# Optimization experiments

Measured on AMD Instinct MI355X. Metric: run time of the kernel, lower is better.

## Reference

```python
import jax, jax.numpy as jnp
import numpy as np

D_MODEL = 1024
NHEAD = 16
HEAD_DIM = D_MODEL // NHEAD


def setup_inputs() -> dict:
    key = jax.random.key(0)
    ks = jax.random.split(key, 9)
    s = 0.02
    x = jax.random.normal(ks[0], (2, 2048, D_MODEL), dtype=jnp.float32)
    Wq = jax.random.normal(ks[1], (D_MODEL, D_MODEL), dtype=jnp.float32) * s
    bq = jnp.zeros((D_MODEL,), jnp.float32)
    Wk = jax.random.normal(ks[2], (D_MODEL, D_MODEL), dtype=jnp.float32) * s
    bk = jnp.zeros((D_MODEL,), jnp.float32)
    Wv = jax.random.normal(ks[3], (D_MODEL, D_MODEL), dtype=jnp.float32) * s
    bv = jnp.zeros((D_MODEL,), jnp.float32)
    Wo = jax.random.normal(ks[4], (D_MODEL, D_MODEL), dtype=jnp.float32) * s
    bo = jnp.zeros((D_MODEL,), jnp.float32)
    return {"x": x, "Wq": Wq, "bq": bq, "Wk": Wk, "bk": bk,
            "Wv": Wv, "bv": bv, "Wo": Wo, "bo": bo}


def _rope(x, sin, cos):
    # x: [B, L, H, Dh]; rotate-half as in the torch module
    half = x.shape[-1] // 2
    x1, x2 = x[..., :half], x[..., half:]
    rotated = jnp.concatenate([-x2, x1], axis=-1)
    return x * cos + rotated * sin


def reference(x, Wq, bq, Wk, bk, Wv, bv, Wo, bo):
    B, L, D = x.shape
    H, Dh = NHEAD, HEAD_DIM
    q = (x @ Wq.T + bq).reshape(B, L, H, Dh)
    k = (x @ Wk.T + bk).reshape(B, L, H, Dh)
    v = (x @ Wv.T + bv).reshape(B, L, H, Dh)

    inv_freq = 1.0 / (10000.0 ** (jnp.arange(0, Dh, 2, dtype=jnp.float32) / Dh))
    t = jnp.arange(L, dtype=jnp.float32)
    freqs = jnp.einsum('i,j->ij', t, inv_freq)          # [L, Dh/2]
    emb = jnp.concatenate([freqs, freqs], axis=-1)      # [L, Dh]
    cos = jnp.cos(emb)[None, :, None, :]
    sin = jnp.sin(emb)[None, :, None, :]

    q = _rope(q, sin, cos)
    k = _rope(k, sin, cos)

    # [B, H, L, L]
    scores = jnp.einsum('bqhd,bkhd->bhqk', q, k) / jnp.sqrt(jnp.float32(Dh))
    attn = jax.nn.softmax(scores, axis=-1)
    # dropout in eval mode = identity (p given as 0.0)
    out = jnp.einsum('bhqk,bkhd->bqhd', attn, v).reshape(B, L, D)
    return out @ Wo.T + bo
```

## Files before the change

kernel.cpp:

```cpp
#include <hip/hip_runtime.h>
#include <math.h>

#define D_MODEL 1024
#define NHEAD 16
#define HEAD_DIM 64
#define L_SEQ 2048
#define BATCH 2
#define M_ROWS 4096
#define SC_Q 0.18033688011112042f

typedef __attribute__((ext_vector_type(8))) short short8;
typedef __attribute__((ext_vector_type(4))) float floatx4;
typedef __attribute__((ext_vector_type(2))) __fp16 half2_t;
typedef __attribute__((ext_vector_type(4))) __fp16 half4_t;
typedef __attribute__((ext_vector_type(8))) __fp16 half8_t;

#if __has_builtin(__builtin_amdgcn_exp2f)
#define EXP2F(x) __builtin_amdgcn_exp2f(x)
#else
#define EXP2F(x) exp2f(x)
#endif

__device__ inline unsigned f2bf_u(float x) {
    unsigned u = __float_as_uint(x);
    return (u + 0x7fffu + ((u >> 16) & 1u)) >> 16;
}

__device__ inline void gl_lds16(const void* g, void* l) {
    __builtin_amdgcn_global_load_lds((const __attribute__((address_space(1))) void*)g,
                                     (__attribute__((address_space(3))) void*)l, 16, 0, 0);
}

__device__ inline void permlane16_swap(unsigned& a, unsigned& b) {
#if __has_builtin(__builtin_amdgcn_permlane16_swap)
    auto r = __builtin_amdgcn_permlane16_swap(a, b, false, false);
    a = r[0];
    b = r[1];
#else
    asm("v_permlane16_swap_b32 %0, %1" : "+v"(a), "+v"(b));
#endif
}

__global__ __launch_bounds__(256) void cvt_all(
    const float* __restrict__ x,  const float* __restrict__ wq,
    const float* __restrict__ wk, const float* __restrict__ wv,
    const float* __restrict__ wo,
    unsigned short* __restrict__ xb,  unsigned short* __restrict__ wqb,
    unsigned short* __restrict__ wkb, unsigned short* __restrict__ wvb,
    unsigned short* __restrict__ wob, float* __restrict__ rt) {
    if (blockIdx.y == 5) {
        for (int idx = blockIdx.x * 256 + threadIdx.x; idx < L_SEQ * 16;
             idx += gridDim.x * 256) {
            int l = idx >> 4, f = idx & 15;
            float if0 = (float)pow(10000.0, -(double)f / 32.0);
            float if1 = (float)pow(10000.0, -(double)(f + 16) / 32.0);
            float s0, c0, s1, c1;
            sincosf((float)l * if0, &s0, &c0);
            sincosf((float)l * if1, &s1, &c1);
            float4 v = {c0, c1, s0, s1};
            *(float4*)(rt + (size_t)idx * 4) = v;
        }
        return;
    }
    const float* s; unsigned short* d; int n;
    switch (blockIdx.y) {
        case 0:  s = x;  d = xb;  n = M_ROWS * D_MODEL; break;
        case 1:  s = wq; d = wqb; n = D_MODEL * D_MODEL; break;
        case 2:  s = wk; d = wkb; n = D_MODEL * D_MODEL; break;
        case 3:  s = wv; d = wvb; n = D_MODEL * D_MODEL; break;
        default: s = wo; d = wob; n = D_MODEL * D_MODEL; break;
    }
    int stride = gridDim.x * 256 * 4;
    for (int i = (blockIdx.x * 256 + threadIdx.x) * 4; i < n; i += stride) {
        float4 v = *(const float4*)(s + i);
        ushort4 o;
        o.x = (unsigned short)f2bf_u(v.x);
        o.y = (unsigned short)f2bf_u(v.y);
        o.z = (unsigned short)f2bf_u(v.z);
        o.w = (unsigned short)f2bf_u(v.w);
        *(ushort4*)(d + i) = o;
    }
}

__global__ __launch_bounds__(256, 3) void gemm_qkv(
    const unsigned short* __restrict__ xb,
    const unsigned short* __restrict__ wqb, const unsigned short* __restrict__ wkb,
    const unsigned short* __restrict__ wvb,
    const float* __restrict__ bq, const float* __restrict__ bk,
    const float* __restrict__ bv, const float* __restrict__ rt,
    unsigned short* __restrict__ qo, unsigned short* __restrict__ ko,
    unsigned short* __restrict__ vo) {
    __shared__ __align__(16) unsigned short As[128 * 64];
    __shared__ __align__(16) unsigned short Bs[128 * 64];

    const int K = D_MODEL;
    const int tid = threadIdx.x;
    const int lane = tid & 63;
    const int w = tid >> 6;
    const int quad = lane >> 4;
    const int wm = (w & 1) * 64;
    const int wn = (w >> 1) * 64;
    const int m0 = blockIdx.x * 128;
    const int n0 = blockIdx.y * 128;

    const unsigned short* Wsel; const float* bsel;
    unsigned short* osel; int mode; float oscale;
    if (blockIdx.z == 0)      { Wsel = wqb; bsel = bq; osel = qo; mode = 1; oscale = SC_Q; }
    else if (blockIdx.z == 1) { Wsel = wkb; bsel = bk; osel = ko; mode = 1; oscale = 1.0f; }
    else                      { Wsel = wvb; bsel = bv; osel = vo; mode = 2; oscale = 1.0f; }

    floatx4 acc[4][4];
#pragma unroll
    for (int i = 0; i < 4; ++i)
#pragma unroll
        for (int j = 0; j < 4; ++j) acc[i][j] = (floatx4){0.f, 0.f, 0.f, 0.f};

    const int sr8 = lane >> 3;
    const int ss8 = lane & 7;
    const unsigned short* Ag = xb + (size_t)m0 * K;
    const unsigned short* Bg = Wsel + (size_t)n0 * K;

    for (int k0 = 0; k0 < K; k0 += 64) {
        __syncthreads();
#pragma unroll
        for (int t = 0; t < 4; ++t) {
            int R0 = t * 32 + w * 8;
            int r = R0 + sr8;
            int c = ss8 ^ (r & 7);
            gl_lds16(Ag + (size_t)r * K + k0 + c * 8, (void*)(As + R0 * 64));
            gl_lds16(Bg + (size_t)r * K + k0 + c * 8, (void*)(Bs + R0 * 64));
        }
        __syncthreads();

#pragma unroll
        for (int ks = 0; ks < 2; ++ks) {
            short8 af[4], bf[4];
#pragma unroll
            for (int mt = 0; mt < 4; ++mt) {
                int ar = wm + mt * 16 + (lane & 15);
                int slot = (ks * 4 + quad) ^ (ar & 7);
                af[mt] = *(const short8*)(As + ar * 64 + slot * 8);
            }
#pragma unroll
            for (int nt = 0; nt < 4; ++nt) {
                int br = wn + nt * 16 + (lane & 15);
                int slot = (ks * 4 + quad) ^ (br & 7);
                bf[nt] = *(const short8*)(Bs + br * 64 + slot * 8);
            }
#pragma unroll
            for (int mt = 0; mt < 4; ++mt)
#pragma unroll
                for (int nt = 0; nt < 4; ++nt)
                    acc[mt][nt] = __builtin_amdgcn_mfma_f32_16x16x32_bf16(
                        af[mt], bf[nt], acc[mt][nt], 0, 0, 0);
        }
    }

#pragma unroll
    for (int nt = 0; nt < 4; ++nt) {
        float bn = bsel[n0 + wn + nt * 16 + (lane & 15)];
#pragma unroll
        for (int mt = 0; mt < 4; ++mt)
#pragma unroll
            for (int i = 0; i < 4; ++i) acc[mt][nt][i] += bn;
    }

    const int h = (n0 + wn) >> 6;

    if (mode == 1) {
#pragma unroll
        for (int mt = 0; mt < 4; ++mt)
#pragma unroll
            for (int i = 0; i < 4; ++i) {
                int m = m0 + wm + mt * 16 + (lane >> 4) * 4 + i;
                int b = m >> 11, l = m & (L_SEQ - 1);
                float4 tc = *(const float4*)(rt + ((size_t)(l * 16 + (lane & 15)) << 2));
#pragma unroll
                for (int nt = 0; nt < 4; ++nt) {
                    int dh = nt * 16 + (lane & 15);
                    float partner = acc[mt][nt ^ 2][i];
                    float rot = (nt < 2) ? -partner : partner;
                    float c = (nt & 1) ? tc.y : tc.x;
                    float s = (nt & 1) ? tc.w : tc.z;
                    float val = (acc[mt][nt][i] * c + rot * s) * oscale;
                    size_t idx = (((size_t)(b * NHEAD + h)) * L_SEQ + l) * HEAD_DIM + dh;
                    osel[idx] = (unsigned short)f2bf_u(val);
                }
            }
    } else {
#pragma unroll
        for (int mt = 0; mt < 4; ++mt)
#pragma unroll
            for (int ih = 0; ih < 4; ih += 2) {
                int m = m0 + wm + mt * 16 + (lane >> 4) * 4 + ih;
                int b = m >> 11, l = m & (L_SEQ - 1);
#pragma unroll
                for (int nt = 0; nt < 4; ++nt) {
                    int dh = nt * 16 + (lane & 15);
                    union { half2_t h; unsigned u; } cv;
                    cv.h = __builtin_amdgcn_cvt_pkrtz(acc[mt][nt][ih], acc[mt][nt][ih + 1]);
                    size_t idx = (((size_t)(b * NHEAD + h)) * HEAD_DIM + dh) * L_SEQ + l;
                    *(unsigned*)(vo + idx) = cv.u;
                }
            }
    }
}

__global__ __launch_bounds__(256) void gemm_out(
    const unsigned short* __restrict__ A, const unsigned short* __restrict__ Wb,
    const float* __restrict__ bias, float* __restrict__ out) {
    __shared__ __align__(16) unsigned short As[64 * 64];
    __shared__ __align__(16) unsigned short Bs[128 * 64];

    const int K = D_MODEL;
    const int tid = threadIdx.x;
    const int lane = tid & 63;
    const int w = tid >> 6;
    const int quad = lane >> 4;
    const int wm = (w & 1) * 32;
    const int wn = (w >> 1) * 64;
    const int m0 = blockIdx.x * 64;
    const int n0 = blockIdx.y * 128;

    floatx4 acc[2][4];
#pragma unroll
    for (int i = 0; i < 2; ++i)
#pragma unroll
        for (int j = 0; j < 4; ++j) acc[i][j] = (floatx4){0.f, 0.f, 0.f, 0.f};

    const int sr8 = lane >> 3;
    const int ss8 = lane & 7;
    const unsigned short* Ag = A + (size_t)m0 * K;
    const unsigned short* Bg = Wb + (size_t)n0 * K;

    for (int k0 = 0; k0 < K; k0 += 64) {
        __syncthreads();
#pragma unroll
        for (int t = 0; t < 2; ++t) {
            int R0 = t * 32 + w * 8;
            int r = R0 + sr8;
            int c = ss8 ^ (r & 7);
            gl_lds16(Ag + (size_t)r * K + k0 + c * 8, (void*)(As + R0 * 64));
        }
#pragma unroll
        for (int t = 0; t < 4; ++t) {
            int R0 = t * 32 + w * 8;
            int r = R0 + sr8;
            int c = ss8 ^ (r & 7);
            gl_lds16(Bg + (size_t)r * K + k0 + c * 8, (void*)(Bs + R0 * 64));
        }
        __syncthreads();

        short8 af[2][2], bf[4][2];
#pragma unroll
        for (int mt = 0; mt < 2; ++mt) {
            int ar = wm + mt * 16 + (lane & 15);
#pragma unroll
            for (int ks = 0; ks < 2; ++ks) {
                int slot = (ks * 4 + quad) ^ (ar & 7);
                af[mt][ks] = *(const short8*)(As + ar * 64 + slot * 8);
            }
        }
#pragma unroll
        for (int nt = 0; nt < 4; ++nt) {
            int br = wn + nt * 16 + (lane & 15);
#pragma unroll
            for (int ks = 0; ks < 2; ++ks) {
                int slot = (ks * 4 + quad) ^ (br & 7);
                bf[nt][ks] = *(const short8*)(Bs + br * 64 + slot * 8);
            }
        }
#pragma unroll
        for (int ks = 0; ks < 2; ++ks)
#pragma unroll
            for (int mt = 0; mt < 2; ++mt)
#pragma unroll
                for (int nt = 0; nt < 4; ++nt)
                    acc[mt][nt] = __builtin_amdgcn_mfma_f32_16x16x32_bf16(
                        af[mt][ks], bf[nt][ks], acc[mt][nt], 0, 0, 0);
    }

#pragma unroll
    for (int nt = 0; nt < 4; ++nt) {
        int n = n0 + wn + nt * 16 + (lane & 15);
        float bn = bias[n];
#pragma unroll
        for (int mt = 0; mt < 2; ++mt)
#pragma unroll
            for (int i = 0; i < 4; ++i) {
                int m = m0 + wm + mt * 16 + (lane >> 4) * 4 + i;
                out[(size_t)m * D_MODEL + n] = acc[mt][nt][i] + bn;
            }
    }
}

__global__ __launch_bounds__(256, 4) void attn_mfma(
    const unsigned short* __restrict__ q, const unsigned short* __restrict__ k,
    const unsigned short* __restrict__ vt,
    unsigned short* __restrict__ ao) {
    __shared__ __align__(16) unsigned short Ks[128 * 64];
    __shared__ __align__(16) unsigned short Vs[64 * 128];

    const int tid = threadIdx.x;
    const int lane = tid & 63;
    const int w = tid >> 6;
    const int quad = lane >> 4;
    const int ln = lane & 15;

    const int GX = L_SEQ / 64;
    int lin = blockIdx.y * GX + blockIdx.x;
    lin = (lin & 7) * 128 + (lin >> 3);
    const int q0 = (lin & (GX - 1)) * 64;
    const int bh = lin >> 5;

    const unsigned short* qb = q + (size_t)bh * L_SEQ * HEAD_DIM;
    const unsigned short* kb = k + (size_t)bh * L_SEQ * HEAD_DIM;
    const unsigned short* vb = vt + (size_t)bh * HEAD_DIM * L_SEQ;

    short8 qf[2];
#pragma unroll
    for (int ks = 0; ks < 2; ++ks)
        qf[ks] = *(const short8*)(
            qb + (size_t)(q0 + w * 16 + ln) * HEAD_DIM + ks * 32 + quad * 8);

    floatx4 o[4];
    floatx4 ls;
    ls = (floatx4){0.f, 0.f, 0.f, 0.f};
#pragma unroll
    for (int j = 0; j < 4; ++j) o[j] = (floatx4){0.f, 0.f, 0.f, 0.f};

    half8_t ones8;
#pragma unroll
    for (int j = 0; j < 8; ++j) ones8[j] = (__fp16)1.0f;

    const int srk = lane >> 3;
    const int ssk = lane & 7;
    const int srv = lane >> 4;
    const int ssv = lane & 15;
    const int pb = ((quad & 1) << 1) | (quad >> 1);

    for (int t = 0; t < L_SEQ / 128; ++t) {
        const int kv0 = t * 128;
        __syncthreads();
#pragma unroll
        for (int tt = 0; tt < 4; ++tt) {
            {
                int R0 = tt * 32 + w * 8;
                int r = R0 + srk;
                int c = ssk ^ (r & 7);
                gl_lds16(kb + (size_t)(kv0 + r) * HEAD_DIM + c * 8, (void*)(Ks + R0 * 64));
            }
            {
                int R0 = tt * 16 + w * 4;
                int r = R0 + srv;
                int c = ssv ^ (r & 15);
                gl_lds16(vb + (size_t)r * L_SEQ + kv0 + c * 8, (void*)(Vs + R0 * 128));
            }
        }
        __syncthreads();

#pragma unroll
        for (int mt2 = 0; mt2 < 4; ++mt2) {
            floatx4 s0 = (floatx4){0.f, 0.f, 0.f, 0.f};
            floatx4 s1 = (floatx4){0.f, 0.f, 0.f, 0.f};
            {
                int ar = mt2 * 32 + ln;
                short8 kf0 = *(const short8*)(Ks + ar * 64 + ((quad) ^ (ar & 7)) * 8);
                short8 kf1 = *(const short8*)(Ks + ar * 64 + ((4 + quad) ^ (ar & 7)) * 8);
                s0 = __builtin_amdgcn_mfma_f32_16x16x32_bf16(kf0, qf[0], s0, 0, 0, 0);
                s0 = __builtin_amdgcn_mfma_f32_16x16x32_bf16(kf1, qf[1], s0, 0, 0, 0);
            }
            {
                int ar = mt2 * 32 + 16 + ln;
                short8 kf0 = *(const short8*)(Ks + ar * 64 + ((quad) ^ (ar & 7)) * 8);
                short8 kf1 = *(const short8*)(Ks + ar * 64 + ((4 + quad) ^ (ar & 7)) * 8);
                s1 = __builtin_amdgcn_mfma_f32_16x16x32_bf16(kf0, qf[0], s1, 0, 0, 0);
                s1 = __builtin_amdgcn_mfma_f32_16x16x32_bf16(kf1, qf[1], s1, 0, 0, 0);
            }

            half8_t vf[4];
#pragma unroll
            for (int ntd = 0; ntd < 4; ++ntd) {
                int row = ntd * 16 + ln;
                int slot = (mt2 * 4 + pb) ^ (row & 15);
                vf[ntd] = *(const half8_t*)(Vs + row * 128 + slot * 8);
            }

            {
                union { half2_t h; unsigned u; } c0l, c0h, c1l, c1h;
                c0l.h = __builtin_amdgcn_cvt_pkrtz(EXP2F(s0[0]), EXP2F(s0[1]));
                c0h.h = __builtin_amdgcn_cvt_pkrtz(EXP2F(s0[2]), EXP2F(s0[3]));
                c1l.h = __builtin_amdgcn_cvt_pkrtz(EXP2F(s1[0]), EXP2F(s1[1]));
                c1h.h = __builtin_amdgcn_cvt_pkrtz(EXP2F(s1[2]), EXP2F(s1[3]));
                unsigned a0 = c0l.u, b0 = c1l.u;
                unsigned a1 = c0h.u, b1 = c1h.u;
                permlane16_swap(a0, b0);
                permlane16_swap(a1, b1);
                union { half8_t h8; unsigned u[4]; } af;
                af.u[0] = a0; af.u[1] = a1; af.u[2] = b0; af.u[3] = b1;

                ls = __builtin_amdgcn_mfma_f32_16x16x32_f16(af.h8, ones8, ls, 0, 0, 0);
#pragma unroll
                for (int ntd = 0; ntd < 4; ++ntd)
                    o[ntd] = __builtin_amdgcn_mfma_f32_16x16x32_f16(
                        af.h8, vf[ntd], o[ntd], 0, 0, 0);
            }
        }
    }

    const int b = bh >> 4, h = bh & (NHEAD - 1);
#pragma unroll
    for (int i = 0; i < 4; ++i) {
        int l = q0 + w * 16 + quad * 4 + i;
        float inv = 1.0f / ls[i];
#pragma unroll
        for (int ntd = 0; ntd < 4; ++ntd) {
            int dh = ntd * 16 + ln;
            size_t idx = ((size_t)b * L_SEQ + l) * D_MODEL + h * HEAD_DIM + dh;
            ao[idx] = (unsigned short)f2bf_u(o[ntd][i] * inv);
        }
    }
}

extern "C" void kernel_launch(void* const* d_in, const int* in_sizes, int n_in,
                              void* d_out, int out_size, void* d_ws, size_t ws_size,
                              hipStream_t stream) {
    const float* x  = (const float*)d_in[0];
    const float* Wq = (const float*)d_in[1];
    const float* bq = (const float*)d_in[2];
    const float* Wk = (const float*)d_in[3];
    const float* bk = (const float*)d_in[4];
    const float* Wv = (const float*)d_in[5];
    const float* bv = (const float*)d_in[6];
    const float* Wo = (const float*)d_in[7];
    const float* bo = (const float*)d_in[8];
    float* outp = (float*)d_out;

    const size_t XE = (size_t)M_ROWS * D_MODEL;
    const size_t WE = (size_t)D_MODEL * D_MODEL;
    unsigned short* wqb = (unsigned short*)d_ws;
    unsigned short* wkb = wqb + WE;
    unsigned short* wvb = wkb + WE;
    unsigned short* wob = wvb + WE;
    unsigned short* qbf = wob + WE;
    unsigned short* kbf = qbf + XE;
    unsigned short* vtb = kbf + XE;
    unsigned short* xb  = vtb + XE;
    unsigned short* aob = xb;
    float* rt    = (float*)(xb + XE);

    cvt_all<<<dim3(1024, 6), 256, 0, stream>>>(x, Wq, Wk, Wv, Wo,
                                               xb, wqb, wkb, wvb, wob, rt);

    gemm_qkv<<<dim3(M_ROWS / 128, D_MODEL / 128, 3), 256, 0, stream>>>(
        xb, wqb, wkb, wvb, bq, bk, bv, rt, qbf, kbf, vtb);

    attn_mfma<<<dim3(L_SEQ / 64, BATCH * NHEAD), 256, 0, stream>>>(
        qbf, kbf, vtb, aob);

    gemm_out<<<dim3(M_ROWS / 64, D_MODEL / 128), 256, 0, stream>>>(aob, wob, bo, outp);
}
```

Measured before the change: 184.4 us.

## Split KV tile across warp pairs with 32-row query tiles and LDS reduction

Each attention warp now handles 32 query rows instead of 16 and processes only half of each 128-key tile, with warp pairs splitting the KV dimension. This halves the K and V LDS fragment reads per query row, since each K and V fragment now feeds two query tiles. The partial outputs and row sums are combined through shared memory at the end. The cost is more accumulator registers, which may limit occupancy under launch_bounds(256,4), plus an extra sync and reduction step.

```diff
diff --git a/kernel.cpp b/kernel.cpp
--- a/kernel.cpp
+++ b/kernel.cpp
@@ -298,14 +298,17 @@
     const unsigned short* __restrict__ q, const unsigned short* __restrict__ k,
     const unsigned short* __restrict__ vt,
     unsigned short* __restrict__ ao) {
-    __shared__ __align__(16) unsigned short Ks[128 * 64];
-    __shared__ __align__(16) unsigned short Vs[64 * 128];
+    __shared__ __align__(16) unsigned short Sh[128 * 64 + 64 * 128];
+    unsigned short* Ks = Sh;
+    unsigned short* Vs = Sh + 128 * 64;
 
     const int tid = threadIdx.x;
     const int lane = tid & 63;
     const int w = tid >> 6;
     const int quad = lane >> 4;
     const int ln = lane & 15;
+    const int qt = w & 1;
+    const int p = w >> 1;
 
     const int GX = L_SEQ / 64;
     int lin = blockIdx.y * GX + blockIdx.x;
@@ -317,17 +320,23 @@
     const unsigned short* kb = k + (size_t)bh * L_SEQ * HEAD_DIM;
     const unsigned short* vb = vt + (size_t)bh * HEAD_DIM * L_SEQ;
 
-    short8 qf[2];
-#pragma unroll
-    for (int ks = 0; ks < 2; ++ks)
-        qf[ks] = *(const short8*)(
-            qb + (size_t)(q0 + w * 16 + ln) * HEAD_DIM + ks * 32 + quad * 8);
-
-    floatx4 o[4];
-    floatx4 ls;
-    ls = (floatx4){0.f, 0.f, 0.f, 0.f};
-#pragma unroll
-    for (int j = 0; j < 4; ++j) o[j] = (floatx4){0.f, 0.f, 0.f, 0.f};
+    short8 qf[2][2];
+#pragma unroll
+    for (int ntq = 0; ntq < 2; ++ntq)
+#pragma unroll
+        for (int ks = 0; ks < 2; ++ks)
+            qf[ntq][ks] = *(const short8*)(
+                qb + (size_t)(q0 + qt * 32 + ntq * 16 + ln) * HEAD_DIM
+                + ks * 32 + quad * 8);
+
+    floatx4 o[2][4];
+    floatx4 ls[2];
+#pragma unroll
+    for (int ntq = 0; ntq < 2; ++ntq) {
+        ls[ntq] = (floatx4){0.f, 0.f, 0.f, 0.f};
+#pragma unroll
+        for (int j = 0; j < 4; ++j) o[ntq][j] = (floatx4){0.f, 0.f, 0.f, 0.f};
+    }
 
     half8_t ones8;
 #pragma unroll
@@ -360,22 +369,23 @@
         __syncthreads();
 
 #pragma unroll
-        for (int mt2 = 0; mt2 < 4; ++mt2) {
-            floatx4 s0 = (floatx4){0.f, 0.f, 0.f, 0.f};
-            floatx4 s1 = (floatx4){0.f, 0.f, 0.f, 0.f};
-            {
-                int ar = mt2 * 32 + ln;
+        for (int mm = 0; mm < 2; ++mm) {
+            const int mt2 = 2 * p + mm;
+            floatx4 s[2][2];
+#pragma unroll
+            for (int c = 0; c < 2; ++c) {
+                int ar = mt2 * 32 + c * 16 + ln;
                 short8 kf0 = *(const short8*)(Ks + ar * 64 + ((quad) ^ (ar & 7)) * 8);
                 short8 kf1 = *(const short8*)(Ks + ar * 64 + ((4 + quad) ^ (ar & 7)) * 8);
-                s0 = __builtin_amdgcn_mfma_f32_16x16x32_bf16(kf0, qf[0], s0, 0, 0, 0);
-                s0 = __builtin_amdgcn_mfma_f32_16x16x32_bf16(kf1, qf[1], s0, 0, 0, 0);
-            }
-            {
-                int ar = mt2 * 32 + 16 + ln;
-                short8 kf0 = *(const short8*)(Ks + ar * 64 + ((quad) ^ (ar & 7)) * 8);
-                short8 kf1 = *(const short8*)(Ks + ar * 64 + ((4 + quad) ^ (ar & 7)) * 8);
-                s1 = __builtin_amdgcn_mfma_f32_16x16x32_bf16(kf0, qf[0], s1, 0, 0, 0);
-                s1 = __builtin_amdgcn_mfma_f32_16x16x32_bf16(kf1, qf[1], s1, 0, 0, 0);
+
+                floatx4 t0 = (floatx4){0.f, 0.f, 0.f, 0.f};
+                floatx4 t1 = (floatx4){0.f, 0.f, 0.f, 0.f};
+                t0 = __builtin_amdgcn_mfma_f32_16x16x32_bf16(kf0, qf[0][0], t0, 0, 0, 0);
+                t0 = __builtin_amdgcn_mfma_f32_16x16x32_bf16(kf1, qf[0][1], t0, 0, 0, 0);
+                t1 = __builtin_amdgcn_mfma_f32_16x16x32_bf16(kf0, qf[1][0], t1, 0, 0, 0);
+                t1 = __builtin_amdgcn_mfma_f32_16x16x32_bf16(kf1, qf[1][1], t1, 0, 0, 0);
+                s[c][0] = t0;
+                s[c][1] = t1;
             }
 
             half8_t vf[4];
@@ -386,12 +396,13 @@
                 vf[ntd] = *(const half8_t*)(Vs + row * 128 + slot * 8);
             }
 
-            {
+#pragma unroll
+            for (int ntq = 0; ntq < 2; ++ntq) {
                 union { half2_t h; unsigned u; } c0l, c0h, c1l, c1h;
-                c0l.h = __builtin_amdgcn_cvt_pkrtz(EXP2F(s0[0]), EXP2F(s0[1]));
-                c0h.h = __builtin_amdgcn_cvt_pkrtz(EXP2F(s0[2]), EXP2F(s0[3]));
-                c1l.h = __builtin_amdgcn_cvt_pkrtz(EXP2F(s1[0]), EXP2F(s1[1]));
-                c1h.h = __builtin_amdgcn_cvt_pkrtz(EXP2F(s1[2]), EXP2F(s1[3]));
+                c0l.h = __builtin_amdgcn_cvt_pkrtz(EXP2F(s[0][ntq][0]), EXP2F(s[0][ntq][1]));
+                c0h.h = __builtin_amdgcn_cvt_pkrtz(EXP2F(s[0][ntq][2]), EXP2F(s[0][ntq][3]));
+                c1l.h = __builtin_amdgcn_cvt_pkrtz(EXP2F(s[1][ntq][0]), EXP2F(s[1][ntq][1]));
+                c1h.h = __builtin_amdgcn_cvt_pkrtz(EXP2F(s[1][ntq][2]), EXP2F(s[1][ntq][3]));
                 unsigned a0 = c0l.u, b0 = c1l.u;
                 unsigned a1 = c0h.u, b1 = c1h.u;
                 permlane16_swap(a0, b0);
@@ -399,26 +410,52 @@
                 union { half8_t h8; unsigned u[4]; } af;
                 af.u[0] = a0; af.u[1] = a1; af.u[2] = b0; af.u[3] = b1;
 
-                ls = __builtin_amdgcn_mfma_f32_16x16x32_f16(af.h8, ones8, ls, 0, 0, 0);
+                ls[ntq] = __builtin_amdgcn_mfma_f32_16x16x32_f16(af.h8, ones8, ls[ntq], 0, 0, 0);
 #pragma unroll
                 for (int ntd = 0; ntd < 4; ++ntd)
-                    o[ntd] = __builtin_amdgcn_mfma_f32_16x16x32_f16(
-                        af.h8, vf[ntd], o[ntd], 0, 0, 0);
-            }
-        }
-    }
-
-    const int b = bh >> 4, h = bh & (NHEAD - 1);
-#pragma unroll
-    for (int i = 0; i < 4; ++i) {
-        int l = q0 + w * 16 + quad * 4 + i;
-        float inv = 1.0f / ls[i];
-#pragma unroll
-        for (int ntd = 0; ntd < 4; ++ntd) {
-            int dh = ntd * 16 + ln;
-            size_t idx = ((size_t)b * L_SEQ + l) * D_MODEL + h * HEAD_DIM + dh;
-            ao[idx] = (unsigned short)f2bf_u(o[ntd][i] * inv);
-        }
+                    o[ntq][ntd] = __builtin_amdgcn_mfma_f32_16x16x32_f16(
+                        af.h8, vf[ntd], o[ntq][ntd], 0, 0, 0);
+            }
+        }
+    }
+
+    __syncthreads();
+    float* cb = (float*)Sh;
+    if (p == 1) {
+        float* dst = cb + (size_t)(qt * 64 + lane) * 40;
+#pragma unroll
+        for (int ntq = 0; ntq < 2; ++ntq) {
+#pragma unroll
+            for (int ntd = 0; ntd < 4; ++ntd)
+                *(floatx4*)(dst + ntq * 20 + ntd * 4) = o[ntq][ntd];
+            *(floatx4*)(dst + ntq * 20 + 16) = ls[ntq];
+        }
+    }
+    __syncthreads();
+    if (p == 0) {
+        const float* src = cb + (size_t)(qt * 64 + lane) * 40;
+#pragma unroll
+        for (int ntq = 0; ntq < 2; ++ntq) {
+#pragma unroll
+            for (int ntd = 0; ntd < 4; ++ntd)
+                o[ntq][ntd] += *(const floatx4*)(src + ntq * 20 + ntd * 4);
+            ls[ntq] += *(const floatx4*)(src + ntq * 20 + 16);
+        }
+
+        const int b = bh >> 4, h = bh & (NHEAD - 1);
+#pragma unroll
+        for (int ntq = 0; ntq < 2; ++ntq)
+#pragma unroll
+            for (int i = 0; i < 4; ++i) {
+                int l = q0 + qt * 32 + ntq * 16 + quad * 4 + i;
+                float inv = 1.0f / ls[ntq][i];
+#pragma unroll
+                for (int ntd = 0; ntd < 4; ++ntd) {
+                    int dh = ntd * 16 + ln;
+                    size_t idx = ((size_t)b * L_SEQ + l) * D_MODEL + h * HEAD_DIM + dh;
+                    ao[idx] = (unsigned short)f2bf_u(o[ntq][ntd][i] * inv);
+                }
+            }
     }
 }
 
```

Measured after the change: 183.0 us. About the same (-0.7%).
